# Performance work log

Hardware: AMD Instinct MI355X
Metric: run time of the kernel (lower is better)

## Reference

```python
import jax, jax.numpy as jnp
import numpy as np

D_MODEL = 1024
N_HEAD = 16
D_FF = 4096
SEQ = 2048
BATCH = 4
EPS = 1e-5


def setup_inputs() -> dict:
    key = jax.random.key(0)
    ks = jax.random.split(key, 10)
    s = 0.02
    return {
        "src": jax.random.normal(ks[0], (SEQ, BATCH, D_MODEL), jnp.float32),
        "padding_mask": jnp.zeros((BATCH, SEQ), jnp.bool_),
        "w_qkv": jax.random.normal(ks[1], (3 * D_MODEL, D_MODEL), jnp.float32) * s,
        "fc_w": jax.random.normal(ks[2], (D_MODEL, D_MODEL), jnp.float32) * s,
        "fc_b": jnp.zeros((D_MODEL,), jnp.float32),
        "w1": jax.random.normal(ks[3], (D_FF, D_MODEL), jnp.float32) * s,
        "b1": jnp.zeros((D_FF,), jnp.float32),
        "w2": jax.random.normal(ks[4], (D_MODEL, D_FF), jnp.float32) * s,
        "b2": jnp.zeros((D_MODEL,), jnp.float32),
        "g1": jnp.ones((D_MODEL,), jnp.float32),
        "be1": jnp.zeros((D_MODEL,), jnp.float32),
        "g2": jnp.ones((D_MODEL,), jnp.float32),
        "be2": jnp.zeros((D_MODEL,), jnp.float32),
    }


def _layer_norm(x, g, b):
    mu = jnp.mean(x, axis=-1, keepdims=True)
    var = jnp.mean(jnp.square(x - mu), axis=-1, keepdims=True)
    return (x - mu) * jax.lax.rsqrt(var + EPS) * g + b


def _mha(src, padding_mask, w_qkv, fc_w, fc_b):
    L, B, D = src.shape
    H = N_HEAD
    dh = D // H
    qkv = jnp.einsum("lbd,ed->lbe", src, w_qkv)  # (L,B,3D)
    q, k, v = jnp.split(qkv, 3, axis=-1)
    # (L, B*H, dh) -> (B*H, L, dh)
    q = q.reshape(L, B * H, dh).transpose(1, 0, 2)
    k = k.reshape(L, B * H, dh).transpose(1, 0, 2)
    v = v.reshape(L, B * H, dh).transpose(1, 0, 2)
    scores = jnp.einsum("nqd,nkd->nqk", q, k) / np.sqrt(dh).astype(np.float32)
    scores = scores.reshape(B, H, L, L)
    scores = jnp.where(padding_mask[:, None, None, :], -jnp.inf, scores)
    attn = jax.nn.softmax(scores, axis=-1).reshape(B * H, L, L)
    out = jnp.einsum("nqk,nkd->nqd", attn, v)  # (B*H, L, dh)
    out = out.transpose(1, 0, 2).reshape(L, B, D)
    return out @ fc_w.T + fc_b


def reference(src, padding_mask, w_qkv, fc_w, fc_b, w1, b1, w2, b2, g1, be1, g2, be2):
    src2 = _mha(src, padding_mask, w_qkv, fc_w, fc_b)
    src = _layer_norm(src + src2, g1, be1)
    h = jax.nn.relu(src @ w1.T + b1)
    src2 = h @ w2.T + b2
    return _layer_norm(src + src2, g2, be2)
```

## Files before the change

kernel.cpp:

```cpp
#include <hip/hip_runtime.h>
#include <cstdint>
#include <cstddef>

typedef __attribute__((ext_vector_type(8))) short bf16x8;
typedef __attribute__((ext_vector_type(4))) float f32x4;
typedef __attribute__((ext_vector_type(16))) float f32x16;

static __device__ __forceinline__ unsigned short f2bf(float f) {
    union { float f; unsigned u; } v; v.f = f;
    unsigned r = v.u + 0x7FFFu + ((v.u >> 16) & 1u);
    return (unsigned short)(r >> 16);
}

static __device__ __forceinline__ void gld_lds16(const void* g, void* l) {
    unsigned loff = (unsigned)(size_t)l;
    loff = (unsigned)__builtin_amdgcn_readfirstlane((int)loff);
    __builtin_amdgcn_global_load_lds(
        (const __attribute__((address_space(1))) unsigned int*)(size_t)g,
        (__attribute__((address_space(3))) unsigned int*)(size_t)loff,
        16, 0, 0);
}

static __device__ __forceinline__ float xhalf_max(float x) {
    float a = x, b = x;
    asm("v_permlane32_swap_b32 %0, %1" : "+v"(a), "+v"(b));
    return fmaxf(a, b);
}
static __device__ __forceinline__ float xhalf_add(float x) {
    float a = x, b = x;
    asm("v_permlane32_swap_b32 %0, %1" : "+v"(a), "+v"(b));
    return a + b;
}
static __device__ __forceinline__ float max3f(float a, float b, float c) {
    float d;
    asm("v_max3_f32 %0, %1, %2, %3" : "=v"(d) : "v"(a), "v"(b), "v"(c));
    return d;
}

__global__ __launch_bounds__(256) void k_cvt(const float* __restrict__ in,
                                             unsigned short* __restrict__ out, int n) {
    int i = (blockIdx.x * 256 + threadIdx.x) * 4;
    if (i >= n) return;
    float4 v = *reinterpret_cast<const float4*>(in + i);
    ushort4 o;
    o.x = f2bf(v.x); o.y = f2bf(v.y); o.z = f2bf(v.z); o.w = f2bf(v.w);
    *reinterpret_cast<ushort4*>(out + i) = o;
}

template<int BM, int MF>
__global__ __launch_bounds__(512, 2) void k_gemm8(
    const unsigned short* __restrict__ A, const unsigned short* __restrict__ W,
    float* __restrict__ Cf, unsigned short* __restrict__ Cb,
    const float* __restrict__ bias,
    int M, int N, int K, int scale_cols, float scale, int relu)
{
    __shared__ unsigned short As[2][BM * 64];
    __shared__ unsigned short Bs[2][256 * 64];
    const int tid = threadIdx.x, wid = tid >> 6, lane = tid & 63;
    const int lr = lane & 15, g16 = (lane >> 4) * 16;
    const int wm = wid >> 2, wn = wid & 3;

    const int nbx = N >> 8;
    const int nwg = gridDim.x;
    const int raw = blockIdx.x;
    const int swz = (raw & 7) * (nwg >> 3) + (raw >> 3);
    const int bm = (swz / nbx) * BM, bn = (swz % nbx) * 256;

    const int rin = tid >> 3;
    const int cole = (((tid & 7) * 16) ^ ((rin & 7) << 4)) >> 1;

    auto STAGE = [&](int bb, int kt1) {
        #pragma unroll
        for (int c = 0; c < BM / 64; ++c)
            gld_lds16(A + (size_t)(bm + c * 64 + rin) * K + kt1 + cole,
                      (char*)As[bb] + c * 8192 + wid * 1024);
        #pragma unroll
        for (int c = 0; c < 4; ++c)
            gld_lds16(W + (size_t)(bn + c * 64 + rin) * K + kt1 + cole,
                      (char*)Bs[bb] + c * 8192 + wid * 1024);
    };

    f32x4 acc[MF][4] = {};

    STAGE(0, 0);
    int cur = 0;

    for (int kt = 0; kt < K; kt += 64) {
        __syncthreads();

        const char* Ab = (const char*)As[cur];
        const char* Bb = (const char*)Bs[cur];
        bf16x8 bfr[4][2];

        #pragma unroll
        for (int p = 0; p < MF / 2; ++p) {
            bf16x8 af[2][2];
            #pragma unroll
            for (int mi = 0; mi < 2; ++mi)
                #pragma unroll
                for (int kk = 0; kk < 2; ++kk) {
                    const int row = wm * (MF * 16) + (2 * p + mi) * 16 + lr;
                    af[mi][kk] = *reinterpret_cast<const bf16x8*>(
                        Ab + row * 128 + ((kk * 64 + g16) ^ ((row & 7) << 4)));
                }
            if (p == 0) {
                #pragma unroll
                for (int n = 0; n < 4; ++n)
                    #pragma unroll
                    for (int kk = 0; kk < 2; ++kk) {
                        const int row = wn * 64 + n * 16 + lr;
                        bfr[n][kk] = *reinterpret_cast<const bf16x8*>(
                            Bb + row * 128 + ((kk * 64 + g16) ^ ((row & 7) << 4)));
                    }
                if (kt + 64 < K) STAGE(cur ^ 1, kt + 64);
            }
            __builtin_amdgcn_s_barrier();
            __builtin_amdgcn_s_setprio(1);
            #pragma unroll
            for (int mi = 0; mi < 2; ++mi)
                #pragma unroll
                for (int n = 0; n < 4; ++n)
                    #pragma unroll
                    for (int kk = 0; kk < 2; ++kk)
                        acc[2 * p + mi][n] = __builtin_amdgcn_mfma_f32_16x16x32_bf16(
                            af[mi][kk], bfr[n][kk], acc[2 * p + mi][n], 0, 0, 0);
            __builtin_amdgcn_s_setprio(0);
            __builtin_amdgcn_s_barrier();
        }
        cur ^= 1;
    }

    #pragma unroll
    for (int m = 0; m < MF; ++m) {
        #pragma unroll
        for (int n = 0; n < 4; ++n) {
            const int col = bn + wn * 64 + n * 16 + lr;
            const float bv = bias ? bias[col] : 0.0f;
            const float sc = (col < scale_cols) ? scale : 1.0f;
            #pragma unroll
            for (int r = 0; r < 4; ++r) {
                const int row = bm + wm * (MF * 16) + m * 16 + (lane >> 4) * 4 + r;
                float v = acc[m][n][r] * sc + bv;
                if (relu) v = fmaxf(v, 0.0f);
                if (Cb) Cb[(size_t)row * N + col] = f2bf(v);
                else    Cf[(size_t)row * N + col] = v;
            }
        }
    }
}

__global__ __launch_bounds__(256) void k_vtrans(
    const unsigned short* __restrict__ qkv, unsigned short* __restrict__ vt)
{
    __shared__ unsigned short T[64][72];
    const int n = blockIdx.y, b = n >> 4, h = n & 15;
    const int l0 = blockIdx.x * 64;
    const int tid = threadIdx.x;
    {
        const int l = tid >> 2, d = (tid & 3) * 16;
        const unsigned short* p = qkv + (size_t)(l0 + l) * 12288 + b * 3072 + 2048 + h * 64 + d;
        *reinterpret_cast<bf16x8*>(&T[l][d])     = *reinterpret_cast<const bf16x8*>(p);
        *reinterpret_cast<bf16x8*>(&T[l][d + 8]) = *reinterpret_cast<const bf16x8*>(p + 8);
    }
    __syncthreads();
    {
        const int d = tid >> 2, lc = (tid & 3) * 16;
        unsigned short tmp[16];
        #pragma unroll
        for (int j = 0; j < 16; ++j) tmp[j] = T[lc + j][d];
        unsigned short* q = vt + ((size_t)n * 64 + d) * 2048 + l0 + lc;
        *reinterpret_cast<bf16x8*>(q)     = *reinterpret_cast<bf16x8*>(tmp);
        *reinterpret_cast<bf16x8*>(q + 8) = *reinterpret_cast<bf16x8*>(tmp + 8);
    }
}

__global__ __launch_bounds__(256) void k_attn(
    const unsigned short* __restrict__ qkv,
    const unsigned short* __restrict__ vt,
    const unsigned char* __restrict__ mask,
    unsigned short* __restrict__ out)
{
    __shared__ unsigned short Ks[2][64 * 64];
    __shared__ unsigned short Vs[2][64 * 64];
    const int tid = threadIdx.x, wid = tid >> 6, lane = tid & 63;
    const int q32 = lane & 31, hi = lane >> 5;
    const int raw = blockIdx.x;
    const int swz = (raw & 7) * 128 + (raw >> 3);
    const int n = swz >> 4, qblk = swz & 15;
    const int b = n >> 4, h = n & 15;
    const int qbase = qblk * 128 + wid * 32;
    const size_t SL = 12288;

    bf16x8 qf[4];
    {
        const unsigned short* qrow = qkv + (size_t)(qbase + q32) * SL + (size_t)b * 3072 + h * 64;
        #pragma unroll
        for (int t = 0; t < 4; ++t)
            qf[t] = *reinterpret_cast<const bf16x8*>(qrow + t * 16 + hi * 8);
    }

    bool anym;
    {
        const uint4* mp = reinterpret_cast<const uint4*>(mask + b * 2048);
        uint4 m0 = mp[lane * 2], m1 = mp[lane * 2 + 1];
        unsigned mo = m0.x | m0.y | m0.z | m0.w | m1.x | m1.y | m1.z | m1.w;
        anym = __any(mo != 0);
    }

    const int sw = (q32 & 7) << 4;
    int koff[4], voff[2][2];
    #pragma unroll
    for (int t = 0; t < 4; ++t) koff[t] = q32 * 128 + ((t * 32 + hi * 16) ^ sw);
    #pragma unroll
    for (int ks = 0; ks < 2; ++ks)
        #pragma unroll
        for (int hf = 0; hf < 2; ++hf)
            voff[ks][hf] = q32 * 128 + ((ks * 64 + hf * 32 + hi * 16) ^ sw);

    const int soff = wid * 1024 + lane * 16;
    const int srow0 = soff >> 7;
    const int sbc0  = (soff & 127) ^ ((srow0 & 7) << 4);
    const int srow1 = (soff + 4096) >> 7;
    const int sbc1  = ((soff + 4096) & 127) ^ ((srow1 & 7) << 4);
    const unsigned short* kgbase = qkv + (size_t)b * 3072 + 1024 + h * 64;
    const unsigned short* vgbase = vt + (size_t)n * 64 * 2048;

    #define STAGE(buf, kt)                                                            \
        do {                                                                          \
            gld_lds16(kgbase + (size_t)((kt) + srow0) * SL + (sbc0 >> 1),             \
                      (char*)Ks[buf] + wid * 1024);                                   \
            gld_lds16(vgbase + (size_t)srow0 * 2048 + (kt) + (sbc0 >> 1),             \
                      (char*)Vs[buf] + wid * 1024);                                   \
            gld_lds16(kgbase + (size_t)((kt) + srow1) * SL + (sbc1 >> 1),             \
                      (char*)Ks[buf] + 4096 + wid * 1024);                            \
            gld_lds16(vgbase + (size_t)srow1 * 2048 + (kt) + (sbc1 >> 1),             \
                      (char*)Vs[buf] + 4096 + wid * 1024);                            \
        } while (0)

    float m_run = -1e30f, l_run = 0.0f;
    f32x16 o0 = {}, o1 = {};

    STAGE(0, 0);
    int cur = 0;

    for (int kt = 0; kt < 2048; kt += 64) {
        __syncthreads();
        if (kt + 64 < 2048) STAGE(cur ^ 1, kt + 64);
        const char* Kb = (const char*)Ks[cur];
        const char* Vb = (const char*)Vs[cur];

        #pragma unroll
        for (int ks = 0; ks < 2; ++ks) {
            f32x16 s = {};
            __builtin_amdgcn_s_setprio(1);
            #pragma unroll
            for (int t = 0; t < 4; ++t) {
                const bf16x8 kf = *reinterpret_cast<const bf16x8*>(Kb + ks * 4096 + koff[t]);
                s = __builtin_amdgcn_mfma_f32_32x32x16_bf16(kf, qf[t], s, 0, 0, 0);
            }
            __builtin_amdgcn_s_setprio(0);

            if (anym) {
                #pragma unroll
                for (int r = 0; r < 16; ++r) {
                    const int kl = (r & 3) + 8 * (r >> 2) + 4 * hi;
                    if (mask[b * 2048 + kt + ks * 32 + kl]) s[r] = -3e8f;
                }
            }

            float pa = max3f(s[0], s[1], s[2]);
            float pb = max3f(s[3], s[4], s[5]);
            float pc = max3f(s[6], s[7], s[8]);
            float pd = max3f(s[9], s[10], s[11]);
            float pe = max3f(s[12], s[13], s[14]);
            pa = max3f(pa, pb, pc);
            pb = max3f(pd, pe, s[15]);
            float pm = xhalf_max(fmaxf(pa, pb));

            if (!__all(pm <= m_run + 8.0f)) {
                const float mnew = fmaxf(m_run, pm);
                const float al = exp2f(m_run - mnew);
                #pragma unroll
                for (int i = 0; i < 16; ++i) { o0[i] *= al; o1[i] *= al; }
                l_run *= al;
                m_run = mnew;
            }

            #pragma unroll
            for (int i = 0; i < 16; ++i) s[i] = exp2f(s[i] - m_run);
            float t8[8], t4[4];
            #pragma unroll
            for (int i = 0; i < 8; ++i) t8[i] = s[i] + s[i + 8];
            #pragma unroll
            for (int i = 0; i < 4; ++i) t4[i] = t8[i] + t8[i + 4];
            l_run += xhalf_add((t4[0] + t4[1]) + (t4[2] + t4[3]));

            unsigned pk[8];
            #pragma unroll
            for (int i = 0; i < 8; ++i)
                asm("v_cvt_pk_bf16_f32 %0, %1, %2" : "=v"(pk[i]) : "v"(s[2 * i]), "v"(s[2 * i + 1]));
            asm("v_permlane32_swap_b32 %0, %1" : "+v"(pk[2]), "+v"(pk[0]));
            asm("v_permlane32_swap_b32 %0, %1" : "+v"(pk[3]), "+v"(pk[1]));
            asm("v_permlane32_swap_b32 %0, %1" : "+v"(pk[6]), "+v"(pk[4]));
            asm("v_permlane32_swap_b32 %0, %1" : "+v"(pk[7]), "+v"(pk[5]));
            union { unsigned w[4]; bf16x8 v; } pb0, pb1;
            pb0.w[0] = pk[0]; pb0.w[1] = pk[1]; pb0.w[2] = pk[2]; pb0.w[3] = pk[3];
            pb1.w[0] = pk[4]; pb1.w[1] = pk[5]; pb1.w[2] = pk[6]; pb1.w[3] = pk[7];

            const bf16x8 v00 = *reinterpret_cast<const bf16x8*>(Vb + voff[ks][0]);
            const bf16x8 v01 = *reinterpret_cast<const bf16x8*>(Vb + voff[ks][1]);
            const bf16x8 v10 = *reinterpret_cast<const bf16x8*>(Vb + 4096 + voff[ks][0]);
            const bf16x8 v11 = *reinterpret_cast<const bf16x8*>(Vb + 4096 + voff[ks][1]);
            __builtin_amdgcn_s_setprio(1);
            o0 = __builtin_amdgcn_mfma_f32_32x32x16_bf16(v00, pb0.v, o0, 0, 0, 0);
            o0 = __builtin_amdgcn_mfma_f32_32x32x16_bf16(v01, pb1.v, o0, 0, 0, 0);
            o1 = __builtin_amdgcn_mfma_f32_32x32x16_bf16(v10, pb0.v, o1, 0, 0, 0);
            o1 = __builtin_amdgcn_mfma_f32_32x32x16_bf16(v11, pb1.v, o1, 0, 0, 0);
            __builtin_amdgcn_s_setprio(0);
        }
        cur ^= 1;
    }
    #undef STAGE

    const float rl = 1.0f / l_run;
    unsigned short* orow = out + ((size_t)(qbase + q32) * 4 + b) * 1024 + h * 64;
    #pragma unroll
    for (int q4 = 0; q4 < 4; ++q4) {
        unsigned w0, w1, w2, w3;
        asm("v_cvt_pk_bf16_f32 %0, %1, %2" : "=v"(w0) : "v"(o0[q4 * 4 + 0] * rl), "v"(o0[q4 * 4 + 1] * rl));
        asm("v_cvt_pk_bf16_f32 %0, %1, %2" : "=v"(w1) : "v"(o0[q4 * 4 + 2] * rl), "v"(o0[q4 * 4 + 3] * rl));
        asm("v_cvt_pk_bf16_f32 %0, %1, %2" : "=v"(w2) : "v"(o1[q4 * 4 + 0] * rl), "v"(o1[q4 * 4 + 1] * rl));
        asm("v_cvt_pk_bf16_f32 %0, %1, %2" : "=v"(w3) : "v"(o1[q4 * 4 + 2] * rl), "v"(o1[q4 * 4 + 3] * rl));
        uint2 ua; ua.x = w0; ua.y = w1;
        uint2 ub; ub.x = w2; ub.y = w3;
        *reinterpret_cast<uint2*>(orow + q4 * 8 + hi * 4)      = ua;
        *reinterpret_cast<uint2*>(orow + 32 + q4 * 8 + hi * 4) = ub;
    }
}

__global__ __launch_bounds__(256) void k_add_ln(
    const float* __restrict__ x, const float* __restrict__ y,
    const float* __restrict__ gamma, const float* __restrict__ beta,
    float* __restrict__ outf, unsigned short* __restrict__ outb)
{
    const int row = blockIdx.x * 4 + (threadIdx.x >> 6);
    const int lane = threadIdx.x & 63;
    const size_t base = (size_t)row * 1024;
    float v[16];
    float s = 0.0f, ss = 0.0f;
    #pragma unroll
    for (int i = 0; i < 4; ++i) {
        const int c = lane * 4 + i * 256;
        float4 a = *reinterpret_cast<const float4*>(x + base + c);
        float4 d = *reinterpret_cast<const float4*>(y + base + c);
        v[i * 4 + 0] = a.x + d.x; v[i * 4 + 1] = a.y + d.y;
        v[i * 4 + 2] = a.z + d.z; v[i * 4 + 3] = a.w + d.w;
        #pragma unroll
        for (int j = 0; j < 4; ++j) { s += v[i * 4 + j]; ss += v[i * 4 + j] * v[i * 4 + j]; }
    }
    #pragma unroll
    for (int o = 1; o < 64; o <<= 1) { s += __shfl_xor(s, o); ss += __shfl_xor(ss, o); }
    const float mu = s * (1.0f / 1024.0f);
    const float var = ss * (1.0f / 1024.0f) - mu * mu;
    const float rstd = rsqrtf(var + 1e-5f);
    #pragma unroll
    for (int i = 0; i < 4; ++i) {
        const int c = lane * 4 + i * 256;
        float4 gq = *reinterpret_cast<const float4*>(gamma + c);
        float4 bq = *reinterpret_cast<const float4*>(beta + c);
        float4 o;
        o.x = (v[i * 4 + 0] - mu) * rstd * gq.x + bq.x;
        o.y = (v[i * 4 + 1] - mu) * rstd * gq.y + bq.y;
        o.z = (v[i * 4 + 2] - mu) * rstd * gq.z + bq.z;
        o.w = (v[i * 4 + 3] - mu) * rstd * gq.w + bq.w;
        *reinterpret_cast<float4*>(outf + base + c) = o;
        if (outb) {
            ushort4 ob;
            ob.x = f2bf(o.x); ob.y = f2bf(o.y); ob.z = f2bf(o.z); ob.w = f2bf(o.w);
            *reinterpret_cast<ushort4*>(outb + base + c) = ob;
        }
    }
}

extern "C" void kernel_launch(void* const* d_in, const int* in_sizes, int n_in,
                              void* d_out, int out_size, void* d_ws, size_t ws_size,
                              hipStream_t stream) {
    const float* src  = (const float*)d_in[0];
    const unsigned char* mask = (const unsigned char*)d_in[1];
    const float* w_qkv = (const float*)d_in[2];
    const float* fc_w = (const float*)d_in[3];
    const float* fc_b = (const float*)d_in[4];
    const float* w1   = (const float*)d_in[5];
    const float* b1   = (const float*)d_in[6];
    const float* w2   = (const float*)d_in[7];
    const float* b2   = (const float*)d_in[8];
    const float* g1   = (const float*)d_in[9];
    const float* be1  = (const float*)d_in[10];
    const float* g2   = (const float*)d_in[11];
    const float* be2  = (const float*)d_in[12];
    float* out = (float*)d_out;

    char* ws = (char*)d_ws;
    size_t o = 0;
    auto take = [&](size_t nbytes) { size_t p = o; o += (nbytes + 255) & ~(size_t)255; return p; };
    unsigned short* wqkv_b = (unsigned short*)(ws + take((size_t)3072 * 1024 * 2));
    unsigned short* fcw_b  = (unsigned short*)(ws + take((size_t)1024 * 1024 * 2));
    unsigned short* w1_b   = (unsigned short*)(ws + take((size_t)4096 * 1024 * 2));
    unsigned short* w2_b   = (unsigned short*)(ws + take((size_t)1024 * 4096 * 2));
    unsigned short* src_b  = (unsigned short*)(ws + take((size_t)8192 * 1024 * 2));
    unsigned short* qkv_b  = (unsigned short*)(ws + take((size_t)8192 * 3072 * 2));
    unsigned short* attn_b = (unsigned short*)(ws + take((size_t)8192 * 1024 * 2));
    float*          x1_f   = (float*)(ws + take((size_t)8192 * 1024 * 4));
    unsigned short* h_b    = (unsigned short*)(ws + take((size_t)8192 * 4096 * 2));
    float*          proj_f = (float*)qkv_b;
    float*          y_f    = (float*)qkv_b;
    unsigned short* x1_b   = src_b;
    unsigned short* vt_b   = h_b;

    k_cvt<<<dim3(3072 * 1024 / 1024), 256, 0, stream>>>(w_qkv, wqkv_b, 3072 * 1024);
    k_cvt<<<dim3(1024 * 1024 / 1024), 256, 0, stream>>>(fc_w, fcw_b, 1024 * 1024);
    k_cvt<<<dim3(4096 * 1024 / 1024), 256, 0, stream>>>(w1, w1_b, 4096 * 1024);
    k_cvt<<<dim3(4096 * 1024 / 1024), 256, 0, stream>>>(w2, w2_b, 4096 * 1024);
    k_cvt<<<dim3(8192 * 1024 / 1024), 256, 0, stream>>>(src, src_b, 8192 * 1024);

    k_gemm8<256, 8><<<dim3((8192 / 256) * (3072 / 256)), 512, 0, stream>>>(
        src_b, wqkv_b, nullptr, qkv_b, nullptr, 8192, 3072, 1024, 1024, 0.18033688011112042f, 0);

    k_vtrans<<<dim3(32, 64), 256, 0, stream>>>(qkv_b, vt_b);

    k_attn<<<dim3(1024), 256, 0, stream>>>(qkv_b, vt_b, mask, attn_b);

    k_gemm8<128, 4><<<dim3((8192 / 128) * (1024 / 256)), 512, 0, stream>>>(
        attn_b, fcw_b, proj_f, nullptr, fc_b, 8192, 1024, 1024, 0, 1.0f, 0);

    k_add_ln<<<dim3(8192 / 4), 256, 0, stream>>>(src, proj_f, g1, be1, x1_f, x1_b);

    k_gemm8<256, 8><<<dim3((8192 / 256) * (4096 / 256)), 512, 0, stream>>>(
        x1_b, w1_b, nullptr, h_b, b1, 8192, 4096, 1024, 0, 1.0f, 1);

    k_gemm8<128, 4><<<dim3((8192 / 128) * (1024 / 256)), 512, 0, stream>>>(
        h_b, w2_b, y_f, nullptr, b2, 8192, 1024, 4096, 0, 1.0f, 0);

    k_add_ln<<<dim3(8192 / 4), 256, 0, stream>>>(x1_f, y_f, g2, be2, out, nullptr);
}
```

Baseline: 466.2 us.

## Prefetch two GEMM stages ahead with vmcnt waits and store projections as bf16

The GEMM main loop now stages both LDS buffers up front and issues the load for tile k+2 after computing tile k. It waits with a partial s_waitcnt vmcnt instead of a full __syncthreads, so global loads have longer to land behind compute. Separately, the attention output projection and FFN second GEMM write bf16 instead of fp32, and the add+LayerNorm kernel reads bf16. This halves that intermediate traffic at the cost of extra rounding before the residual add.

```diff
diff --git a/kernel.cpp b/kernel.cpp
--- a/kernel.cpp
+++ b/kernel.cpp
@@ -10,6 +10,9 @@
     union { float f; unsigned u; } v; v.f = f;
     unsigned r = v.u + 0x7FFFu + ((v.u >> 16) & 1u);
     return (unsigned short)(r >> 16);
+}
+static __device__ __forceinline__ float bf2f(unsigned short u) {
+    union { unsigned u; float f; } v; v.u = ((unsigned)u) << 16; return v.f;
 }
 
 static __device__ __forceinline__ void gld_lds16(const void* g, void* l) {
@@ -83,10 +86,18 @@
     f32x4 acc[MF][4] = {};
 
     STAGE(0, 0);
+    STAGE(1, 64);
     int cur = 0;
 
     for (int kt = 0; kt < K; kt += 64) {
-        __syncthreads();
+        if (kt + 64 < K) {
+            if constexpr (BM == 256) asm volatile("s_waitcnt vmcnt(8)" ::: "memory");
+            else                     asm volatile("s_waitcnt vmcnt(6)" ::: "memory");
+        } else {
+            asm volatile("s_waitcnt vmcnt(0)" ::: "memory");
+        }
+        __builtin_amdgcn_s_barrier();
+        __builtin_amdgcn_sched_barrier(0);
 
         const char* Ab = (const char*)As[cur];
         const char* Bb = (const char*)Bs[cur];
@@ -112,7 +123,6 @@
                         bfr[n][kk] = *reinterpret_cast<const bf16x8*>(
                             Bb + row * 128 + ((kk * 64 + g16) ^ ((row & 7) << 4)));
                     }
-                if (kt + 64 < K) STAGE(cur ^ 1, kt + 64);
             }
             __builtin_amdgcn_s_barrier();
             __builtin_amdgcn_s_setprio(1);
@@ -127,6 +137,7 @@
             __builtin_amdgcn_s_setprio(0);
             __builtin_amdgcn_s_barrier();
         }
+        if (kt + 128 < K) STAGE(cur, kt + 128);
         cur ^= 1;
     }
 
@@ -339,7 +350,7 @@
 }
 
 __global__ __launch_bounds__(256) void k_add_ln(
-    const float* __restrict__ x, const float* __restrict__ y,
+    const float* __restrict__ x, const unsigned short* __restrict__ y,
     const float* __restrict__ gamma, const float* __restrict__ beta,
     float* __restrict__ outf, unsigned short* __restrict__ outb)
 {
@@ -352,9 +363,9 @@
     for (int i = 0; i < 4; ++i) {
         const int c = lane * 4 + i * 256;
         float4 a = *reinterpret_cast<const float4*>(x + base + c);
-        float4 d = *reinterpret_cast<const float4*>(y + base + c);
-        v[i * 4 + 0] = a.x + d.x; v[i * 4 + 1] = a.y + d.y;
-        v[i * 4 + 2] = a.z + d.z; v[i * 4 + 3] = a.w + d.w;
+        ushort4 d = *reinterpret_cast<const ushort4*>(y + base + c);
+        v[i * 4 + 0] = a.x + bf2f(d.x); v[i * 4 + 1] = a.y + bf2f(d.y);
+        v[i * 4 + 2] = a.z + bf2f(d.z); v[i * 4 + 3] = a.w + bf2f(d.w);
         #pragma unroll
         for (int j = 0; j < 4; ++j) { s += v[i * 4 + j]; ss += v[i * 4 + j] * v[i * 4 + j]; }
     }
@@ -412,8 +423,8 @@
     unsigned short* attn_b = (unsigned short*)(ws + take((size_t)8192 * 1024 * 2));
     float*          x1_f   = (float*)(ws + take((size_t)8192 * 1024 * 4));
     unsigned short* h_b    = (unsigned short*)(ws + take((size_t)8192 * 4096 * 2));
-    float*          proj_f = (float*)qkv_b;
-    float*          y_f    = (float*)qkv_b;
+    unsigned short* proj_b = qkv_b;
+    unsigned short* y_b    = qkv_b;
     unsigned short* x1_b   = src_b;
     unsigned short* vt_b   = h_b;
 
@@ -431,15 +442,15 @@
     k_attn<<<dim3(1024), 256, 0, stream>>>(qkv_b, vt_b, mask, attn_b);
 
     k_gemm8<128, 4><<<dim3((8192 / 128) * (1024 / 256)), 512, 0, stream>>>(
-        attn_b, fcw_b, proj_f, nullptr, fc_b, 8192, 1024, 1024, 0, 1.0f, 0);
-
-    k_add_ln<<<dim3(8192 / 4), 256, 0, stream>>>(src, proj_f, g1, be1, x1_f, x1_b);
+        attn_b, fcw_b, nullptr, proj_b, fc_b, 8192, 1024, 1024, 0, 1.0f, 0);
+
+    k_add_ln<<<dim3(8192 / 4), 256, 0, stream>>>(src, proj_b, g1, be1, x1_f, x1_b);
 
     k_gemm8<256, 8><<<dim3((8192 / 256) * (4096 / 256)), 512, 0, stream>>>(
         x1_b, w1_b, nullptr, h_b, b1, 8192, 4096, 1024, 0, 1.0f, 1);
 
     k_gemm8<128, 4><<<dim3((8192 / 128) * (1024 / 256)), 512, 0, stream>>>(
-        h_b, w2_b, y_f, nullptr, b2, 8192, 1024, 4096, 0, 1.0f, 0);
-
-    k_add_ln<<<dim3(8192 / 4), 256, 0, stream>>>(x1_f, y_f, g2, be2, out, nullptr);
-}
+        h_b, w2_b, nullptr, y_b, b2, 8192, 1024, 4096, 0, 1.0f, 0);
+
+    k_add_ln<<<dim3(8192 / 4), 256, 0, stream>>>(x1_f, y_b, g2, be2, out, nullptr);
+}
```

Measured after the change: 461.6 us. No clear change (-1.0%).
